# Kernel tuning notes

Hardware: AMD Instinct MI355X
Metric: run time of the kernel (lower is better)

Reference implementation:

```python
import jax, jax.numpy as jnp
import numpy as np

B, D, C, L, H = 4096, 768, 512, 32, 256
E = C * L  # total flattened extension embeddings

def _l2norm(x, eps=1e-12):
    n = jnp.sqrt(jnp.sum(x * x, axis=-1, keepdims=True))
    return x / jnp.maximum(n, eps)

def setup_inputs() -> dict:
    key = jax.random.key(0)
    ks = jax.random.split(key, 8)
    text_feat = jax.random.normal(ks[0], (B, D), dtype=jnp.float32)
    img_feat = jax.random.normal(ks[1], (B, D), dtype=jnp.float32)
    ext_embs = _l2norm(jax.random.normal(ks[2], (E, D), dtype=jnp.float32))
    concept_names = _l2norm(jax.random.normal(ks[3], (C, D), dtype=jnp.float32))
    # each concept has exactly L extension embeddings; sorted segment ids
    segment_ids = jnp.repeat(jnp.arange(C, dtype=jnp.int32), L)
    W1 = jax.random.normal(ks[4], (C + D, H), dtype=jnp.float32) * (1.0 / np.sqrt(C + D))
    b1 = jnp.zeros((H,), dtype=jnp.float32)
    W2 = jax.random.normal(ks[5], (H, C), dtype=jnp.float32) * (1.0 / np.sqrt(H))
    b2 = jnp.zeros((C,), dtype=jnp.float32)
    alpha = jnp.float32(0.5)
    temperature = jnp.float32(0.07)
    return {"text_feat": text_feat, "img_feat": img_feat, "ext_embs": ext_embs,
            "segment_ids": segment_ids, "concept_names": concept_names,
            "W1": W1, "b1": b1, "W2": W2, "b2": b2,
            "alpha": alpha, "temperature": temperature}

def reference(text_feat, img_feat, ext_embs, segment_ids, concept_names,
              W1, b1, W2, b2, alpha, temperature):
    # query = normalize(text + img)
    q = _l2norm(text_feat + img_feat)                      # [B, D]
    # ragged per-concept max similarity: one big GEMM + segmented max
    sim = jnp.einsum('bd,ed->be', q, ext_embs)            # [B, E]
    prior = jax.ops.segment_max(sim.T, segment_ids,
                                num_segments=C,
                                indices_are_sorted=True).T  # [B, C]
    # small MLP -> temperature softmax -> weighted concept sum
    h = jax.nn.relu(jnp.concatenate([prior, q], axis=-1) @ W1 + b1)  # [B, H]
    logits = h @ W2 + b2                                   # [B, C]
    weights = jax.nn.softmax(logits / temperature, axis=-1)
    dyn_prompt = weights @ concept_names                   # [B, D]
    combined = text_feat + alpha * dyn_prompt
    return _l2norm(combined)
```

## Files before the change

kernel.cpp:

```cpp
#include <hip/hip_runtime.h>
#include <hip/hip_bf16.h>

typedef unsigned short bfu;
typedef __attribute__((ext_vector_type(4))) float f32x4;
typedef __attribute__((ext_vector_type(8))) short bf16x8;
typedef __attribute__((ext_vector_type(4))) int i32x4;
typedef __attribute__((ext_vector_type(8))) int i32x8;

__device__ __forceinline__ unsigned short f2bf(float f) {
    unsigned int u = __float_as_uint(f);
    u += 0x7FFFu + ((u >> 16) & 1u);
    return (unsigned short)(u >> 16);
}

__device__ __forceinline__ unsigned pack_fp8x4(float a, float b, float c, float d) {
    int u = __builtin_amdgcn_cvt_pk_fp8_f32(a, b, 0, false);
    u = __builtin_amdgcn_cvt_pk_fp8_f32(c, d, u, true);
    return (unsigned)u;
}

__device__ __forceinline__ float block_sum256(float v, float* sm) {
    #pragma unroll
    for (int off = 32; off; off >>= 1) v += __shfl_xor(v, off);
    int w = threadIdx.x >> 6;
    if ((threadIdx.x & 63) == 0) sm[w] = v;
    __syncthreads();
    float r = sm[0] + sm[1] + sm[2] + sm[3];
    __syncthreads();
    return r;
}

__device__ __forceinline__ float block_max256(float v, float* sm) {
    #pragma unroll
    for (int off = 32; off; off >>= 1) v = fmaxf(v, __shfl_xor(v, off));
    int w = threadIdx.x >> 6;
    if ((threadIdx.x & 63) == 0) sm[w] = v;
    __syncthreads();
    float r = fmaxf(fmaxf(sm[0], sm[1]), fmaxf(sm[2], sm[3]));
    __syncthreads();
    return r;
}

__global__ __launch_bounds__(256) void prep_kernel(const float* __restrict__ text,
                                                   const float* __restrict__ img,
                                                   bfu* __restrict__ X,
                                                   unsigned* __restrict__ Q8,
                                                   const float* __restrict__ ext,
                                                   unsigned* __restrict__ E8,
                                                   const float* __restrict__ W1, bfu* __restrict__ W1t,
                                                   const float* __restrict__ W2, bfu* __restrict__ W2t,
                                                   const float* __restrict__ cn, bfu* __restrict__ cnt) {
    __shared__ float sm[4];
    int b = blockIdx.x, t = threadIdx.x;
    if (b < 4096) {
        int row = b;
        float4 v = {0.f, 0.f, 0.f, 0.f};
        if (t < 192) {
            float4 a = ((const float4*)(text + (size_t)row * 768))[t];
            float4 c = ((const float4*)(img + (size_t)row * 768))[t];
            v.x = a.x + c.x; v.y = a.y + c.y; v.z = a.z + c.z; v.w = a.w + c.w;
        }
        float ss = v.x * v.x + v.y * v.y + v.z * v.z + v.w * v.w;
        float tot = block_sum256(ss, sm);
        float inv = 1.0f / fmaxf(sqrtf(tot), 1e-12f);
        if (t < 192) {
            ushort4 o = make_ushort4(f2bf(v.x * inv), f2bf(v.y * inv), f2bf(v.z * inv), f2bf(v.w * inv));
            ((ushort4*)(X + (size_t)row * 1280 + 512))[t] = o;
            float s16 = inv * 16.0f;
            Q8[(size_t)row * 192 + t] = pack_fp8x4(v.x * s16, v.y * s16, v.z * s16, v.w * s16);
        }
    } else if (b < 16384) {
        int i = (b - 4096) * 256 + t;
        float4 v = ((const float4*)ext)[i];
        E8[i] = pack_fp8x4(v.x * 16.0f, v.y * 16.0f, v.z * 16.0f, v.w * 16.0f);
    } else if (b < 17664) {
        int idx = (b - 16384) * 256 + t;
        int c = idx / 1280, r = idx - c * 1280;
        W1t[idx] = f2bf(W1[(size_t)r * 256 + c]);
    } else if (b < 18176) {
        int idx = (b - 17664) * 256 + t;
        int c = idx / 256, r = idx - c * 256;
        W2t[idx] = f2bf(W2[(size_t)r * 512 + c]);
    } else {
        int idx = (b - 18176) * 256 + t;
        int c = idx / 512, r = idx - c * 512;
        cnt[idx] = f2bf(cn[(size_t)r * 768 + c]);
    }
}

__device__ __forceinline__ i32x8 ld_frag8(const char* s, int row, int lq) {
    const int r7 = row & 7;
    i32x4 lo = *(const i32x4*)(s + row * 128 + ((((lq << 1))     ^ r7) << 4));
    i32x4 hi = *(const i32x4*)(s + row * 128 + ((((lq << 1) | 1) ^ r7) << 4));
    i32x8 v;
    v[0] = lo[0]; v[1] = lo[1]; v[2] = lo[2]; v[3] = lo[3];
    v[4] = hi[0]; v[5] = hi[1]; v[6] = hi[2]; v[7] = hi[3];
    return v;
}

__global__ __launch_bounds__(512) void sim_segmax_kernel(const unsigned char* __restrict__ Q8,
                                                         const unsigned char* __restrict__ E8,
                                                         bfu* __restrict__ X) {
    __shared__ __align__(16) char sA[128 * 128];
    __shared__ __align__(16) char sB[128 * 128];
    int bm = blockIdx.x & 31;
    int bn = blockIdx.x >> 5;
    int m0 = bm * 128, n0 = bn * 128;
    const int t = threadIdx.x, lane = t & 63, wv = t >> 6;
    const int wm = (wv >> 2) << 6;
    const int wn = (wv & 3) << 5;
    const int lr = lane & 15, lq = lane >> 4;

    f32x4 zero = {0.f, 0.f, 0.f, 0.f};
    f32x4 acc[4][2];
    #pragma unroll
    for (int i = 0; i < 4; ++i)
        #pragma unroll
        for (int j = 0; j < 2; ++j) acc[i][j] = zero;

    i32x4 ra[2], rb[2];
    auto ldg = [&](int k0) {
        #pragma unroll
        for (int i = 0; i < 2; ++i) {
            int idx = i * 512 + t;
            int row = idx >> 3, cg = idx & 7;
            ra[i] = *(const i32x4*)(Q8 + (size_t)(m0 + row) * 768 + k0 + (cg << 4));
            rb[i] = *(const i32x4*)(E8 + (size_t)(n0 + row) * 768 + k0 + (cg << 4));
        }
    };
    auto st_lds = [&]() {
        #pragma unroll
        for (int i = 0; i < 2; ++i) {
            int idx = i * 512 + t;
            int row = idx >> 3, cg = idx & 7, cs = cg ^ (row & 7);
            *(i32x4*)(sA + (row * 8 + cs) * 16) = ra[i];
            *(i32x4*)(sB + (row * 8 + cs) * 16) = rb[i];
        }
    };

    ldg(0);
    for (int kk = 0; kk < 6; ++kk) {
        if (kk) __syncthreads();
        st_lds();
        __syncthreads();
        if (kk + 1 < 6) ldg((kk + 1) * 128);
        i32x8 af[4], bf8[2];
        #pragma unroll
        for (int f = 0; f < 4; ++f)
            af[f] = ld_frag8(sA, wm + f * 16 + lr, lq);
        #pragma unroll
        for (int j = 0; j < 2; ++j)
            bf8[j] = ld_frag8(sB, wn + j * 16 + lr, lq);
        #pragma unroll
        for (int i = 0; i < 4; ++i)
            #pragma unroll
            for (int j = 0; j < 2; ++j)
                acc[i][j] = __builtin_amdgcn_mfma_scale_f32_16x16x128_f8f6f4(
                    af[i], bf8[j], acc[i][j], 0, 0, 0, 0x7F7F7F7F, 0, 0x7F7F7F7F);
    }

    const float sc = 0.00390625f;
    const int g = (n0 + wn) >> 5;
    #pragma unroll
    for (int i = 0; i < 4; ++i) {
        #pragma unroll
        for (int r = 0; r < 4; ++r) {
            float v = fmaxf(acc[i][0][r], acc[i][1][r]);
            #pragma unroll
            for (int off = 8; off; off >>= 1)
                v = fmaxf(v, __shfl_xor(v, off));
            if (lr == 0) {
                int row = m0 + wm + i * 16 + lq * 4 + r;
                X[(size_t)row * 1280 + g] = f2bf(v * sc);
            }
        }
    }
}

template <int BM>
__device__ __forceinline__ void gemm_mainloop(const bfu* A, const bfu* B, int K,
                                              int lda, int ldb, int m0, int n0,
                                              short* sA, short* sB, f32x4 acc[BM / 32][4]) {
    const int t = threadIdx.x, lane = t & 63, wv = t >> 6;
    const int wm = (wv >> 1) * (BM / 2), wn = (wv & 1) << 6;
    const int lr = lane & 15, lq = lane >> 4;

    i32x4 ra[BM / 32], rb[4];
    auto ldg = [&](int k0) {
        #pragma unroll
        for (int i = 0; i < BM / 32; ++i) {
            int idx = i * 256 + t;
            int row = idx >> 3, cg = idx & 7;
            ra[i] = *(const i32x4*)(A + (size_t)(m0 + row) * lda + k0 + (cg << 3));
        }
        #pragma unroll
        for (int i = 0; i < 4; ++i) {
            int idx = i * 256 + t;
            int row = idx >> 3, cg = idx & 7;
            rb[i] = *(const i32x4*)(B + (size_t)(n0 + row) * ldb + k0 + (cg << 3));
        }
    };
    auto st_lds = [&]() {
        #pragma unroll
        for (int i = 0; i < BM / 32; ++i) {
            int idx = i * 256 + t;
            int row = idx >> 3, cg = idx & 7, cs = cg ^ (row & 7);
            *(i32x4*)(sA + row * 64 + cs * 8) = ra[i];
        }
        #pragma unroll
        for (int i = 0; i < 4; ++i) {
            int idx = i * 256 + t;
            int row = idx >> 3, cg = idx & 7, cs = cg ^ (row & 7);
            *(i32x4*)(sB + row * 64 + cs * 8) = rb[i];
        }
    };

    const int NIT = K >> 6;
    ldg(0);
    for (int kk = 0; kk < NIT; ++kk) {
        if (kk) __syncthreads();
        st_lds();
        __syncthreads();
        if (kk + 1 < NIT) ldg((kk + 1) * 64);
        #pragma unroll
        for (int ks = 0; ks < 2; ++ks) {
            bf16x8 af[BM / 32], bfr[4];
            #pragma unroll
            for (int f = 0; f < BM / 32; ++f) {
                int mrow = wm + f * 16 + lr;
                int c = ks * 4 + lq;
                af[f] = *(const bf16x8*)(sA + mrow * 64 + ((c ^ (mrow & 7)) << 3));
            }
            #pragma unroll
            for (int f = 0; f < 4; ++f) {
                int nrow = wn + f * 16 + lr;
                int c = ks * 4 + lq;
                bfr[f] = *(const bf16x8*)(sB + nrow * 64 + ((c ^ (nrow & 7)) << 3));
            }
            #pragma unroll
            for (int i = 0; i < BM / 32; ++i)
                #pragma unroll
                for (int j = 0; j < 4; ++j)
                    acc[i][j] = __builtin_amdgcn_mfma_f32_16x16x32_bf16(af[i], bfr[j], acc[i][j], 0, 0, 0);
        }
    }
}

template <int EPI, int BM>
__global__ __launch_bounds__(256) void gemm_kernel(const bfu* __restrict__ A,
                                                   const bfu* __restrict__ B,
                                                   const float* __restrict__ bias,
                                                   void* __restrict__ out,
                                                   int K, int lda, int ldb, int N, int ntN) {
    __shared__ __align__(16) short sA[BM * 64];
    __shared__ __align__(16) short sB[128 * 64];
    int bm = blockIdx.x / ntN, bn = blockIdx.x - bm * ntN;
    int m0 = bm * BM, n0 = bn * 128;
    f32x4 zero = {0.f, 0.f, 0.f, 0.f};
    f32x4 acc[BM / 32][4];
    #pragma unroll
    for (int i = 0; i < BM / 32; ++i)
        #pragma unroll
        for (int j = 0; j < 4; ++j) acc[i][j] = zero;

    gemm_mainloop<BM>(A, B, K, lda, ldb, m0, n0, sA, sB, acc);

    const int t = threadIdx.x, lane = t & 63, wv = t >> 6;
    const int wm = (wv >> 1) * (BM / 2), wn = (wv & 1) << 6;
    const int lr = lane & 15, lq = lane >> 4;
    #pragma unroll
    for (int j = 0; j < 4; ++j) {
        int col = n0 + wn + j * 16 + lr;
        float bv = (EPI >= 1) ? bias[col] : 0.0f;
        #pragma unroll
        for (int i = 0; i < BM / 32; ++i) {
            #pragma unroll
            for (int r = 0; r < 4; ++r) {
                int row = m0 + wm + i * 16 + lq * 4 + r;
                float v = acc[i][j][r] + bv;
                if (EPI == 1) {
                    v = fmaxf(v, 0.0f);
                    ((bfu*)out)[(size_t)row * N + col] = f2bf(v);
                } else {
                    ((float*)out)[(size_t)row * N + col] = v;
                }
            }
        }
    }
}

__global__ __launch_bounds__(256) void softmax_kernel(const float* __restrict__ logits,
                                                      const float* __restrict__ temp,
                                                      bfu* __restrict__ wout) {
    __shared__ float sm[4];
    int row = blockIdx.x, t = threadIdx.x;
    float invT = 1.0f / temp[0];
    float l0 = logits[(size_t)row * 512 + t];
    float l1 = logits[(size_t)row * 512 + 256 + t];
    float m = block_max256(fmaxf(l0, l1), sm);
    float e0 = __expf((l0 - m) * invT);
    float e1 = __expf((l1 - m) * invT);
    float s = block_sum256(e0 + e1, sm);
    float inv = 1.0f / s;
    wout[(size_t)row * 512 + t]       = f2bf(e0 * inv);
    wout[(size_t)row * 512 + 256 + t] = f2bf(e1 * inv);
}

__global__ __launch_bounds__(256) void final_kernel(const float* __restrict__ text,
                                                    const float* __restrict__ dyn,
                                                    const float* __restrict__ alpha,
                                                    float* __restrict__ out) {
    __shared__ float sm[4];
    int row = blockIdx.x, t = threadIdx.x;
    float a = alpha[0];
    float v[3]; float ss = 0.f;
    #pragma unroll
    for (int i = 0; i < 3; ++i) {
        size_t o = (size_t)row * 768 + t + 256 * i;
        v[i] = text[o] + a * dyn[o];
        ss += v[i] * v[i];
    }
    float tot = block_sum256(ss, sm);
    float inv = 1.0f / fmaxf(sqrtf(tot), 1e-12f);
    #pragma unroll
    for (int i = 0; i < 3; ++i)
        out[(size_t)row * 768 + t + 256 * i] = v[i] * inv;
}

extern "C" void kernel_launch(void* const* d_in, const int* in_sizes, int n_in,
                              void* d_out, int out_size, void* d_ws, size_t ws_size,
                              hipStream_t stream) {
    const float* text  = (const float*)d_in[0];
    const float* img   = (const float*)d_in[1];
    const float* ext   = (const float*)d_in[2];
    const float* cn    = (const float*)d_in[4];
    const float* W1    = (const float*)d_in[5];
    const float* b1    = (const float*)d_in[6];
    const float* W2    = (const float*)d_in[7];
    const float* b2    = (const float*)d_in[8];
    const float* alpha = (const float*)d_in[9];
    const float* temp  = (const float*)d_in[10];
    float* out = (float*)d_out;

    char* p = (char*)d_ws;
    auto carve = [&](size_t bytes) -> char* {
        char* r = p; p += (bytes + 255) & ~(size_t)255; return r;
    };
    unsigned char* E8 = (unsigned char*)carve((size_t)16384 * 768);
    unsigned char* Q8 = (unsigned char*)carve((size_t)4096 * 768);
    bfu*   X      = (bfu*)carve((size_t)4096 * 1280 * 2);
    bfu*   W1t    = (bfu*)carve((size_t)256 * 1280 * 2);
    bfu*   W2t    = (bfu*)carve((size_t)512 * 256 * 2);
    bfu*   cnt    = (bfu*)carve((size_t)768 * 512 * 2);
    bfu*   Hm     = (bfu*)carve((size_t)4096 * 256 * 2);
    float* logits = (float*)carve((size_t)4096 * 512 * 4);
    bfu*   wts    = (bfu*)carve((size_t)4096 * 512 * 2);
    float* dyn    = (float*)carve((size_t)4096 * 768 * 4);

    prep_kernel<<<19712, 256, 0, stream>>>(text, img, X, (unsigned*)Q8,
                                           ext, (unsigned*)E8, W1, W1t, W2, W2t, cn, cnt);
    sim_segmax_kernel<<<4096, 512, 0, stream>>>(Q8, E8, X);
    gemm_kernel<1, 64><<<64 * 2, 256, 0, stream>>>(X, W1t, b1, (void*)Hm, 1280, 1280, 1280, 256, 2);
    gemm_kernel<2, 64><<<64 * 4, 256, 0, stream>>>(Hm, W2t, b2, (void*)logits, 256, 256, 256, 512, 4);
    softmax_kernel<<<4096, 256, 0, stream>>>(logits, temp, wts);
    gemm_kernel<0, 64><<<64 * 6, 256, 0, stream>>>(wts, cnt, nullptr, (void*)dyn, 512, 512, 512, 768, 6);
    final_kernel<<<4096, 256, 0, stream>>>(text, dyn, alpha, out);
}
```

Measured before the change: 285.0 us.

## Enlarge sim GEMM tiles to 256x256 with double-buffered direct global-to-LDS loads

Rewrites the FP8 similarity and segment-max GEMM to use 256x256 block tiles, so each wave computes 128x64 and the grid drops to 1024 blocks. Loads now go straight from global memory into LDS through global_load_lds with pre-swizzled source addresses, into double-buffered shared memory. Prefetch of the next K slice is interleaved with the MFMA phases, using barriers and setprio. This raises data reuse and overlaps memory with compute, at the cost of 128KB of LDS per block, more accumulator registers and lower occupancy.

```diff
diff --git a/kernel.cpp b/kernel.cpp
--- a/kernel.cpp
+++ b/kernel.cpp
@@ -17,6 +17,12 @@
     int u = __builtin_amdgcn_cvt_pk_fp8_f32(a, b, 0, false);
     u = __builtin_amdgcn_cvt_pk_fp8_f32(c, d, u, true);
     return (unsigned)u;
+}
+
+__device__ __forceinline__ void gload_lds16(const void* g, void* l) {
+    __builtin_amdgcn_global_load_lds(
+        (const __attribute__((address_space(1))) unsigned int*)g,
+        (__attribute__((address_space(3))) unsigned int*)l, 16, 0, 0);
 }
 
 __device__ __forceinline__ float block_sum256(float v, float* sm) {
@@ -98,80 +104,97 @@
     return v;
 }
 
-__global__ __launch_bounds__(512) void sim_segmax_kernel(const unsigned char* __restrict__ Q8,
-                                                         const unsigned char* __restrict__ E8,
-                                                         bfu* __restrict__ X) {
-    __shared__ __align__(16) char sA[128 * 128];
-    __shared__ __align__(16) char sB[128 * 128];
-    int bm = blockIdx.x & 31;
-    int bn = blockIdx.x >> 5;
-    int m0 = bm * 128, n0 = bn * 128;
+__global__ __launch_bounds__(512, 2) void sim_segmax_kernel(const unsigned char* __restrict__ Q8,
+                                                            const unsigned char* __restrict__ E8,
+                                                            bfu* __restrict__ X) {
+    __shared__ __align__(16) char sA[2][256 * 128];
+    __shared__ __align__(16) char sB[2][256 * 128];
+    const int bm = blockIdx.x & 15;
+    const int bn = blockIdx.x >> 4;
+    const int m0 = bm << 8, n0 = bn << 8;
     const int t = threadIdx.x, lane = t & 63, wv = t >> 6;
-    const int wm = (wv >> 2) << 6;
-    const int wn = (wv & 3) << 5;
+    const int wm = (wv >> 2) << 7;
+    const int wn = (wv & 3) << 6;
     const int lr = lane & 15, lq = lane >> 4;
 
     f32x4 zero = {0.f, 0.f, 0.f, 0.f};
-    f32x4 acc[4][2];
-    #pragma unroll
-    for (int i = 0; i < 4; ++i)
-        #pragma unroll
-        for (int j = 0; j < 2; ++j) acc[i][j] = zero;
-
-    i32x4 ra[2], rb[2];
-    auto ldg = [&](int k0) {
-        #pragma unroll
-        for (int i = 0; i < 2; ++i) {
-            int idx = i * 512 + t;
-            int row = idx >> 3, cg = idx & 7;
-            ra[i] = *(const i32x4*)(Q8 + (size_t)(m0 + row) * 768 + k0 + (cg << 4));
-            rb[i] = *(const i32x4*)(E8 + (size_t)(n0 + row) * 768 + k0 + (cg << 4));
-        }
-    };
-    auto st_lds = [&]() {
-        #pragma unroll
-        for (int i = 0; i < 2; ++i) {
-            int idx = i * 512 + t;
-            int row = idx >> 3, cg = idx & 7, cs = cg ^ (row & 7);
-            *(i32x4*)(sA + (row * 8 + cs) * 16) = ra[i];
-            *(i32x4*)(sB + (row * 8 + cs) * 16) = rb[i];
-        }
-    };
-
-    ldg(0);
+    f32x4 acc[8][4];
+    #pragma unroll
+    for (int i = 0; i < 8; ++i)
+        #pragma unroll
+        for (int j = 0; j < 4; ++j) acc[i][j] = zero;
+
+    auto stageA = [&](char* buf, int k0, int i) {
+        int idx = (i << 9) + t;
+        int row = idx >> 3, c = idx & 7;
+        int cs = c ^ (row & 7);
+        gload_lds16(Q8 + (size_t)(m0 + row) * 768 + k0 + (cs << 4),
+                    buf + (((i << 9) + (wv << 6)) << 4));
+    };
+    auto stageB = [&](char* buf, int k0, int i) {
+        int idx = (i << 9) + t;
+        int row = idx >> 3, c = idx & 7;
+        int cs = c ^ (row & 7);
+        gload_lds16(E8 + (size_t)(n0 + row) * 768 + k0 + (cs << 4),
+                    buf + (((i << 9) + (wv << 6)) << 4));
+    };
+
+    #pragma unroll
+    for (int i = 0; i < 4; ++i) { stageA(sA[0], 0, i); stageB(sB[0], 0, i); }
+    __syncthreads();
+
     for (int kk = 0; kk < 6; ++kk) {
         if (kk) __syncthreads();
-        st_lds();
-        __syncthreads();
-        if (kk + 1 < 6) ldg((kk + 1) * 128);
-        i32x8 af[4], bf8[2];
-        #pragma unroll
-        for (int f = 0; f < 4; ++f)
-            af[f] = ld_frag8(sA, wm + f * 16 + lr, lq);
-        #pragma unroll
-        for (int j = 0; j < 2; ++j)
-            bf8[j] = ld_frag8(sB, wn + j * 16 + lr, lq);
-        #pragma unroll
-        for (int i = 0; i < 4; ++i)
-            #pragma unroll
-            for (int j = 0; j < 2; ++j)
-                acc[i][j] = __builtin_amdgcn_mfma_scale_f32_16x16x128_f8f6f4(
-                    af[i], bf8[j], acc[i][j], 0, 0, 0, 0x7F7F7F7F, 0, 0x7F7F7F7F);
+        char* bufA = sA[kk & 1];
+        char* bufB = sB[kk & 1];
+        char* nxA  = sA[(kk & 1) ^ 1];
+        char* nxB  = sB[(kk & 1) ^ 1];
+        const int k0n = (kk + 1) << 7;
+        const bool pf = (kk < 5);
+        i32x8 bf[4];
+        #pragma unroll
+        for (int p = 0; p < 4; ++p) {
+            if (p == 0) {
+                #pragma unroll
+                for (int j = 0; j < 4; ++j)
+                    bf[j] = ld_frag8(bufB, wn + j * 16 + lr, lq);
+            }
+            i32x8 af[2];
+            #pragma unroll
+            for (int e = 0; e < 2; ++e)
+                af[e] = ld_frag8(bufA, wm + (2 * p + e) * 16 + lr, lq);
+            if (pf) { stageA(nxA, k0n, p); stageB(nxB, k0n, p); }
+            __builtin_amdgcn_s_barrier();
+            asm volatile("s_waitcnt lgkmcnt(0)" ::: "memory");
+            __builtin_amdgcn_sched_barrier(0);
+            __builtin_amdgcn_s_setprio(1);
+            #pragma unroll
+            for (int e = 0; e < 2; ++e)
+                #pragma unroll
+                for (int j = 0; j < 4; ++j)
+                    acc[2 * p + e][j] = __builtin_amdgcn_mfma_scale_f32_16x16x128_f8f6f4(
+                        af[e], bf[j], acc[2 * p + e][j], 0, 0, 0, 0x7F7F7F7F, 0, 0x7F7F7F7F);
+            __builtin_amdgcn_s_setprio(0);
+            __builtin_amdgcn_s_barrier();
+        }
     }
 
     const float sc = 0.00390625f;
-    const int g = (n0 + wn) >> 5;
-    #pragma unroll
-    for (int i = 0; i < 4; ++i) {
-        #pragma unroll
-        for (int r = 0; r < 4; ++r) {
-            float v = fmaxf(acc[i][0][r], acc[i][1][r]);
-            #pragma unroll
-            for (int off = 8; off; off >>= 1)
-                v = fmaxf(v, __shfl_xor(v, off));
-            if (lr == 0) {
-                int row = m0 + wm + i * 16 + lq * 4 + r;
-                X[(size_t)row * 1280 + g] = f2bf(v * sc);
+    const int gbase = (n0 + wn) >> 5;
+    #pragma unroll
+    for (int g = 0; g < 2; ++g) {
+        #pragma unroll
+        for (int i = 0; i < 8; ++i) {
+            #pragma unroll
+            for (int r = 0; r < 4; ++r) {
+                float v = fmaxf(acc[i][2 * g][r], acc[i][2 * g + 1][r]);
+                #pragma unroll
+                for (int off = 8; off; off >>= 1)
+                    v = fmaxf(v, __shfl_xor(v, off));
+                if (lr == 0) {
+                    int row = m0 + wm + i * 16 + lq * 4 + r;
+                    X[(size_t)row * 1280 + gbase + g] = f2bf(v * sc);
+                }
             }
         }
     }
@@ -359,7 +382,7 @@
 
     prep_kernel<<<19712, 256, 0, stream>>>(text, img, X, (unsigned*)Q8,
                                            ext, (unsigned*)E8, W1, W1t, W2, W2t, cn, cnt);
-    sim_segmax_kernel<<<4096, 512, 0, stream>>>(Q8, E8, X);
+    sim_segmax_kernel<<<1024, 512, 0, stream>>>(Q8, E8, X);
     gemm_kernel<1, 64><<<64 * 2, 256, 0, stream>>>(X, W1t, b1, (void*)Hm, 1280, 1280, 1280, 256, 2);
     gemm_kernel<2, 64><<<64 * 4, 256, 0, stream>>>(Hm, W2t, b2, (void*)logits, 256, 256, 256, 512, 4);
     softmax_kernel<<<4096, 256, 0, stream>>>(logits, temp, wts);
```

Result: slower. 497.0 us (+74.4%).
